# Performance work log

Measured on AMD Instinct MI355X. Metric: run time of the kernel, lower is better.

## Reference

```python
import jax, jax.numpy as jnp
import numpy as np

STFT = 1024
SEQ = 256
CTRL = 32
DEPTH = 3
RATIO = 0.5
BATCH = 64


def _layer_sizes(nin, nout, depth, ratio):
    sizes = []
    for i in range(depth + 1):
        f = i / depth
        lin = nin + (nout - nin) * f
        geo = nin * (nout / nin) ** f
        sizes.append(int(round((1 - ratio) * lin + ratio * geo)))
    sizes[0], sizes[-1] = nin, nout
    return sizes


def _mlp(h, Ws, bs):
    # Linear layers with ReLU between hidden layers, linear final layer.
    n = len(Ws)
    for i in range(n):
        h = h @ Ws[i] + bs[i]
        if i < n - 1:
            h = jax.nn.relu(h)
    return h


def setup_inputs() -> dict:
    key = jax.random.key(0)
    keys = jax.random.split(key, 1 + 4 * DEPTH)
    inp = {"x": jax.random.normal(keys[0], (BATCH, STFT, SEQ), dtype=jnp.float32)}
    enc_sizes = _layer_sizes(1 + 2 * STFT, CTRL, DEPTH, RATIO)
    dec_sizes = _layer_sizes(1 + STFT + CTRL, STFT, DEPTH, RATIO)
    k = 1
    for i in range(DEPTH):
        fan_in = enc_sizes[i]
        inp[f"enc_W{i+1}"] = jax.random.normal(keys[k], (enc_sizes[i], enc_sizes[i + 1]), dtype=jnp.float32) / np.sqrt(fan_in); k += 1
        inp[f"enc_b{i+1}"] = jax.random.normal(keys[k], (enc_sizes[i + 1],), dtype=jnp.float32) * 0.01; k += 1
    for i in range(DEPTH):
        fan_in = dec_sizes[i]
        inp[f"dec_W{i+1}"] = jax.random.normal(keys[k], (dec_sizes[i], dec_sizes[i + 1]), dtype=jnp.float32) / np.sqrt(fan_in); k += 1
        inp[f"dec_b{i+1}"] = jax.random.normal(keys[k], (dec_sizes[i + 1],), dtype=jnp.float32) * 0.01; k += 1
    return inp


def _forward(x, encW, encB, decW, decB):
    B, S, T = x.shape  # [batch, stft_buckets, seq]
    # ---- encode (parallel across t: prev_stft is just the shifted input) ----
    xt = jnp.transpose(x, (0, 2, 1))                       # [B, T, S]
    prev = jnp.concatenate([jnp.zeros((B, 1, S), x.dtype), xt[:, :-1, :]], axis=1)
    tcol = (jnp.arange(T, dtype=x.dtype) / T)[None, :, None]
    tcol = jnp.broadcast_to(tcol, (B, T, 1))
    combined = jnp.concatenate([prev, xt, tcol], axis=-1)  # [B, T, 2S+1]
    controls = _mlp(combined, encW, encB)                  # [B, T, CTRL]
    # ---- decode (true sequential dependency -> scan) ----
    ctrl_t = jnp.transpose(controls, (1, 0, 2))            # [T, B, CTRL]
    tvals = jnp.arange(T, dtype=x.dtype) / T

    def step(prev_stft, xs):
        c, tv = xs
        tc = jnp.broadcast_to(tv, (B, 1))
        comb = jnp.concatenate([c, prev_stft, tc], axis=1)  # [B, CTRL+S+1]
        out = _mlp(comb, decW, decB)                        # [B, S]
        return out, out

    _, recon = jax.lax.scan(step, jnp.zeros((B, S), x.dtype), (ctrl_t, tvals))
    return jnp.transpose(recon, (1, 2, 0))                  # [B, S, T]


def reference(x, enc_W1, enc_b1, enc_W2, enc_b2, enc_W3, enc_b3,
              dec_W1, dec_b1, dec_W2, dec_b2, dec_W3, dec_b3):
    encW = [enc_W1, enc_W2, enc_W3]
    encB = [enc_b1, enc_b2, enc_b3]
    decW = [dec_W1, dec_W2, dec_W3]
    decB = [dec_b1, dec_b2, dec_b3]
    return _forward(x, encW, encB, decW, decB)
```

## Files before the change

### kernel.cpp

```cpp
#include <hip/hip_runtime.h>
#include <cstdint>
#include <cstddef>


#define TT 256
#define BB 64
#define SS 1024

#define EK1 2049
#define EN1 944
#define EN2 416
#define EN3 32

#define DN1 1046
#define DN2 1035
#define DN3 1024

#define KP1 1060
#define KP2 1048
#define KP3 1036
#define NQ1 265
#define NQ2 262
#define NQ3 259
#define WROWS1 1048
#define WROWS2 1040
#define WROWS3 1028

#define OFF_XT    ((size_t)0)
#define OFF_WT1   ((size_t)0)
#define OFF_WT2   ((size_t)1110880)
#define OFF_WT3   ((size_t)2200800)
#define OFF_H1S   ((size_t)3266048)
#define OFF_H2S   ((size_t)20436480)
#define OFF_E1    ((size_t)16777216)
#define OFF_E2    ((size_t)(OFF_E1 + 15466496))
#define OFF_COMB  ((size_t)(OFF_E2 + 6815744))
#define OFF_BAR   ((size_t)(OFF_COMB + 17434880))

#define COMB_SLOT (265 * 256)
#define H1_SLOT   (262 * 256)
#define H2_SLOT   (259 * 256)

typedef unsigned uint4v __attribute__((ext_vector_type(4)));

__global__ void zero_init(float* __restrict__ p, size_t n) {
  size_t i = (size_t)blockIdx.x * blockDim.x + threadIdx.x;
  size_t stride = (size_t)gridDim.x * blockDim.x;
  for (; i < n; i += stride) p[i] = 0.f;
}

__global__ void transpose_x(const float* __restrict__ x, float* __restrict__ xt) {
  __shared__ float tile[32][33];
  int b = blockIdx.z;
  int s0 = blockIdx.x << 5;
  int t0 = blockIdx.y << 5;
  int lt = threadIdx.x & 31;
  int ls = threadIdx.x >> 5;
  const float* xp = x + (size_t)b * SS * TT;
#pragma unroll
  for (int i = 0; i < 4; i++) {
    int s = s0 + ls + (i << 3);
    tile[ls + (i << 3)][lt] = xp[(size_t)s * TT + t0 + lt];
  }
  __syncthreads();
  float* xtp = xt + (size_t)b * TT * SS;
#pragma unroll
  for (int i = 0; i < 4; i++) {
    int t = t0 + ls + (i << 3);
    xtp[(size_t)t * SS + s0 + lt] = tile[lt][ls + (i << 3)];
  }
}

__global__ void transpose_w(const float* __restrict__ W, float* __restrict__ WT,
                            int K, int N, int KPAD, int NCP) {
  __shared__ float tl[32][33];
  int c0 = blockIdx.x << 5, k0 = blockIdx.y << 5;
  int lx = threadIdx.x & 31, ly = threadIdx.x >> 5;
#pragma unroll
  for (int i = 0; i < 4; i++) {
    int k = k0 + ly + (i << 3);
    int c = c0 + lx;
    tl[ly + (i << 3)][lx] = (k < K && c < N) ? W[(size_t)k * N + c] : 0.f;
  }
  __syncthreads();
#pragma unroll
  for (int i = 0; i < 4; i++) {
    int c = c0 + ly + (i << 3);
    int k = k0 + lx;
    if (c < NCP && k < KPAD) WT[(size_t)c * KPAD + k] = tl[lx][ly + (i << 3)];
  }
}

__global__ void init_tail(float* __restrict__ comb) {
  int i = blockIdx.x * blockDim.x + threadIdx.x;
  int t = i >> 6, r = i & 63;
  float4 v;
  v.x = (float)t * (1.f / 256.f);
  v.y = v.z = v.w = 0.f;
  *(float4*)(comb + ((size_t)t * 265 + 264) * 256 + (r << 2)) = v;
}

__device__ inline float4 e1_fetch(const float* __restrict__ xt, int m, int kg) {
  float4 z; z.x = z.y = z.z = z.w = 0.f;
  int t = m & 255;
  if (kg < 1024) {
    if (t == 0) return z;
    return *(const float4*)(xt + (((size_t)(m - 1)) << 10) + kg);
  } else if (kg < 2048) {
    return *(const float4*)(xt + (((size_t)m) << 10) + (kg - 1024));
  } else if (kg == 2048) {
    z.x = (float)t * (1.0f / 256.0f);
    return z;
  }
  return z;
}

template <int AMODE, bool RELU, bool SCATTER>
__global__ __launch_bounds__(256, 2) void gemm_enc(
    const float* __restrict__ A, const float* __restrict__ Bw,
    const float* __restrict__ bias, float* __restrict__ C, int K, int N) {
  __shared__ float As[16][132];
  __shared__ float Bs[16][68];
  const int tid = threadIdx.x;
  const int m0 = blockIdx.x << 7;
  const int n0 = blockIdx.y << 6;
  const int rr = tid >> 4;
  const int cc = tid & 15;
  float acc[8][4];
#pragma unroll
  for (int i = 0; i < 8; i++)
#pragma unroll
    for (int j = 0; j < 4; j++) acc[i][j] = 0.f;

  const int ar = tid >> 2;
  const int akq = (tid & 3) << 2;
  const int bk = tid >> 4;
  const int bn = (tid & 15) << 2;

  for (int k0 = 0; k0 < K; k0 += 16) {
#pragma unroll
    for (int p = 0; p < 2; p++) {
      int m = m0 + ar + (p << 6);
      float4 v;
      if (AMODE == 1) v = e1_fetch(A, m, k0 + akq);
      else            v = *(const float4*)(A + (size_t)m * K + k0 + akq);
      As[akq + 0][ar + (p << 6)] = v.x;
      As[akq + 1][ar + (p << 6)] = v.y;
      As[akq + 2][ar + (p << 6)] = v.z;
      As[akq + 3][ar + (p << 6)] = v.w;
    }
    {
      float4 v; v.x = v.y = v.z = v.w = 0.f;
      if ((k0 + bk) < K && (n0 + bn) < N)
        v = *(const float4*)(Bw + (size_t)(k0 + bk) * N + n0 + bn);
      *(float4*)&Bs[bk][bn] = v;
    }
    __syncthreads();
#pragma unroll
    for (int kk = 0; kk < 16; kk++) {
      float a[8], b4[4];
      *(float4*)&a[0] = *(const float4*)&As[kk][rr << 3];
      *(float4*)&a[4] = *(const float4*)&As[kk][(rr << 3) + 4];
      *(float4*)&b4[0] = *(const float4*)&Bs[kk][cc << 2];
#pragma unroll
      for (int i = 0; i < 8; i++)
#pragma unroll
        for (int j = 0; j < 4; j++) acc[i][j] += a[i] * b4[j];
    }
    __syncthreads();
  }

  if (!SCATTER) {
#pragma unroll
    for (int i = 0; i < 8; i++) {
      int m = m0 + (rr << 3) + i;
      int n = n0 + (cc << 2);
      if (n + 3 < N) {
        float4 o;
        o.x = acc[i][0] + bias[n + 0];
        o.y = acc[i][1] + bias[n + 1];
        o.z = acc[i][2] + bias[n + 2];
        o.w = acc[i][3] + bias[n + 3];
        if (RELU) {
          o.x = fmaxf(o.x, 0.f); o.y = fmaxf(o.y, 0.f);
          o.z = fmaxf(o.z, 0.f); o.w = fmaxf(o.w, 0.f);
        }
        *(float4*)(C + (size_t)m * N + n) = o;
      } else {
#pragma unroll
        for (int j = 0; j < 4; j++) {
          if (n + j < N) {
            float v = acc[i][j] + bias[n + j];
            if (RELU) v = fmaxf(v, 0.f);
            C[(size_t)m * N + n + j] = v;
          }
        }
      }
    }
  } else {
#pragma unroll
    for (int i = 0; i < 8; i++) {
      int m = m0 + (rr << 3) + i;
      int t = m & 255, b = m >> 8;
#pragma unroll
      for (int j = 0; j < 4; j++) {
        int n = n0 + (cc << 2) + j;
        if (n < EN3)
          C[((size_t)t * 265 + (n >> 2)) * 256 + (b << 2) + (n & 3)] = acc[i][j] + bias[n];
      }
    }
  }
}

__device__ inline void gbar(unsigned* __restrict__ bar, unsigned gen, int w) {
  __syncthreads();
  if (threadIdx.x == 0)
    __hip_atomic_store(bar + w, gen, __ATOMIC_RELAXED, __HIP_MEMORY_SCOPE_AGENT);
  if (threadIdx.x < 64) {
    const unsigned* fp = bar + (threadIdx.x << 2);
    for (;;) {
      uint4v f;
      asm volatile(
          "global_load_dwordx4 %0, %1, off sc0 sc1\n\t"
          "s_waitcnt vmcnt(0)"
          : "=v"(f) : "v"(fp));
      if (__all(f.x >= gen && f.y >= gen && f.z >= gen && f.w >= gen)) break;
      __builtin_amdgcn_s_sleep(1);
    }
  }
  __syncthreads();
}

#define DEC_FMA(av, jj)                                              \
  do {                                                               \
    const float* wq = w0 + ((jj) << 2);                              \
    _Pragma("unroll") for (int c = 0; c < NCM; c++) {                \
      float4 wv = *(const float4*)(wq + (size_t)c * KPAD);           \
      acc[c] = fmaf((av).x, wv.x, acc[c]);                           \
      acc[c] = fmaf((av).y, wv.y, acc[c]);                           \
      acc[c] = fmaf((av).z, wv.z, acc[c]);                           \
      acc[c] = fmaf((av).w, wv.w, acc[c]);                           \
    }                                                                \
  } while (0)

template <int NQ, int KPAD, bool RELU, int NCM>
__device__ __forceinline__ void dec_phase(
    const float* __restrict__ actb, const float* __restrict__ wt,
    const float* __restrict__ bias, float* __restrict__ outb, int outk_off,
    int nc, int colbase, int r, int q, float* __restrict__ red, int tid) {
  float acc[NCM];
#pragma unroll
  for (int c = 0; c < NCM; c++) acc[c] = 0.f;
  const float* w0 = wt + (size_t)colbase * KPAD;
  const float* ab = actb + (r << 2);
#pragma unroll 4
  for (int j = q; j < NQ; j += 8) {
    float4 a = *(const float4*)(ab + (j << 8));
    DEC_FMA(a, j);
  }

  float* rp = red + tid * 9;
#pragma unroll
  for (int c = 0; c < NCM; c++) rp[c] = acc[c];
  __syncthreads();
  if (tid < (nc << 6)) {
    int rr = tid / nc;
    int cc = tid - rr * nc;
    float s = 0.f;
#pragma unroll
    for (int q2 = 0; q2 < 8; q2++) s += red[((q2 << 6) + rr) * 9 + cc];
    s += bias[colbase + cc];
    if (RELU) s = fmaxf(s, 0.f);
    int kk = outk_off + colbase + cc;
    __hip_atomic_store(outb + ((size_t)(kk >> 2) << 8) + (rr << 2) + (kk & 3), s,
                       __ATOMIC_RELAXED, __HIP_MEMORY_SCOPE_AGENT);
  }
}

__global__ __launch_bounds__(512, 1) void decoder_kernel(
    const float* __restrict__ wt1, const float* __restrict__ b1,
    const float* __restrict__ wt2, const float* __restrict__ b2,
    const float* __restrict__ wt3, const float* __restrict__ b3,
    float* __restrict__ comb, float* __restrict__ h1s, float* __restrict__ h2s,
    unsigned* __restrict__ bar) {
  __shared__ float red[512 * 9];
  const int tid = threadIdx.x;
  const int w = blockIdx.x;
  const int r = tid & 63;
  const int q = __builtin_amdgcn_readfirstlane(tid >> 6);

  const int nc1 = (w < 22) ? 5 : 4;
  const int cb1 = (w < 22) ? w * 5 : 110 + (w - 22) * 4;
  const int nc2 = (w < 11) ? 5 : 4;
  const int cb2 = (w < 11) ? w * 5 : 55 + (w - 11) * 4;
  const int cb3 = w << 2;

  unsigned gen = 0;
  for (int t = 0; t < TT; t++) {
    gen++; gbar(bar, gen, w);
    dec_phase<NQ1, KP1, true, 5>(comb + (size_t)t * COMB_SLOT, wt1, b1,
                                 h1s + (size_t)t * H1_SLOT, 0,
                                 nc1, cb1, r, q, red, tid);
    gen++; gbar(bar, gen, w);
    dec_phase<NQ2, KP2, true, 5>(h1s + (size_t)t * H1_SLOT, wt2, b2,
                                 h2s + (size_t)t * H2_SLOT, 0,
                                 nc2, cb2, r, q, red, tid);
    gen++; gbar(bar, gen, w);
    dec_phase<NQ3, KP3, false, 4>(h2s + (size_t)t * H2_SLOT, wt3, b3,
                                  comb + (size_t)(t + 1) * COMB_SLOT, 32,
                                  4, cb3, r, q, red, tid);
  }
}

__global__ void permute_out2(const float* __restrict__ comb, float* __restrict__ out) {
  __shared__ float tl[64 * 261];
  int Q = blockIdx.x;
  int t0 = blockIdx.y << 6;
  int tid = threadIdx.x;
  int r = tid & 63, ts = tid >> 6;
#pragma unroll
  for (int i = 0; i < 16; i++) {
    int tt = (i << 2) + ts;
    float4 v = *(const float4*)(comb + ((size_t)(t0 + tt + 1) * 265 + 8 + Q) * 256 + (r << 2));
    float* p = &tl[r * 261];
    p[tt] = v.x; p[65 + tt] = v.y; p[130 + tt] = v.z; p[195 + tt] = v.w;
  }
  __syncthreads();
  int kk = tid & 3, r2 = tid >> 2;
  const float* p = &tl[r2 * 261 + kk * 65];
  float* o = out + ((size_t)r2 * 1024 + (Q << 2) + kk) * 256 + t0;
#pragma unroll
  for (int i = 0; i < 16; i++) {
    int b = i << 2;
    float4 v;
    v.x = p[b]; v.y = p[b + 1]; v.z = p[b + 2]; v.w = p[b + 3];
    *(float4*)(o + b) = v;
  }
}

extern "C" void kernel_launch(void* const* d_in, const int* in_sizes, int n_in,
                              void* d_out, int out_size, void* d_ws, size_t ws_size,
                              hipStream_t stream) {
  (void)in_sizes; (void)n_in; (void)out_size; (void)ws_size;
  const float* x   = (const float*)d_in[0];
  const float* eW1 = (const float*)d_in[1];
  const float* eb1 = (const float*)d_in[2];
  const float* eW2 = (const float*)d_in[3];
  const float* eb2 = (const float*)d_in[4];
  const float* eW3 = (const float*)d_in[5];
  const float* eb3 = (const float*)d_in[6];
  const float* dW1 = (const float*)d_in[7];
  const float* db1 = (const float*)d_in[8];
  const float* dW2 = (const float*)d_in[9];
  const float* db2 = (const float*)d_in[10];
  const float* dW3 = (const float*)d_in[11];
  const float* db3 = (const float*)d_in[12];

  float* ws    = (float*)d_ws;
  float* xt    = ws + OFF_XT;
  float* wt1p  = ws + OFF_WT1;
  float* wt2p  = ws + OFF_WT2;
  float* wt3p  = ws + OFF_WT3;
  float* h1sp  = ws + OFF_H1S;
  float* h2sp  = ws + OFF_H2S;
  float* e1p   = ws + OFF_E1;
  float* e2p   = ws + OFF_E2;
  float* combp = ws + OFF_COMB;
  unsigned* barp = (unsigned*)(ws + OFF_BAR);

  zero_init<<<dim3(64), dim3(256), 0, stream>>>(combp, (size_t)COMB_SLOT);
  zero_init<<<dim3(1), dim3(256), 0, stream>>>((float*)barp, (size_t)2048);

  transpose_x<<<dim3(32, 8, 64), dim3(256), 0, stream>>>(x, xt);

  gemm_enc<1, true,  false><<<dim3(128, 15), dim3(256), 0, stream>>>(xt,  eW1, eb1, e1p, EK1, EN1);
  gemm_enc<0, true,  false><<<dim3(128, 7),  dim3(256), 0, stream>>>(e1p, eW2, eb2, e2p, EN1, EN2);
  gemm_enc<0, false, true ><<<dim3(128, 1),  dim3(256), 0, stream>>>(e2p, eW3, eb3, combp, EN2, EN3);

  transpose_w<<<dim3(33, 34), dim3(256), 0, stream>>>(dW1, wt1p, 1057, DN1, KP1, WROWS1);
  transpose_w<<<dim3(33, 33), dim3(256), 0, stream>>>(dW2, wt2p, 1046, DN2, KP2, WROWS2);
  transpose_w<<<dim3(33, 33), dim3(256), 0, stream>>>(dW3, wt3p, 1035, DN3, KP3, WROWS3);
  init_tail<<<dim3(64), dim3(256), 0, stream>>>(combp);

  const float *a0 = wt1p, *a1 = db1, *a2 = wt2p, *a3 = db2, *a4 = wt3p, *a5 = db3;
  float *r0 = combp, *r1 = h1sp, *r2 = h2sp;
  unsigned* r3 = barp;
  void* kargs[] = {&a0, &a1, &a2, &a3, &a4, &a5, &r0, &r1, &r2, &r3};
  hipLaunchCooperativeKernel((void*)decoder_kernel, dim3(256), dim3(512), kargs,
                             0, stream);

  permute_out2<<<dim3(256, 4), dim3(256), 0, stream>>>(combp, (float*)d_out);
}
```

Baseline: 8.992 ms.

## Repartition decoder work into batch-group by column tiles with LDS-staged activations

```diff
diff --git a/kernel.cpp b/kernel.cpp
--- a/kernel.cpp
+++ b/kernel.cpp
@@ -231,48 +231,68 @@
   __syncthreads();
 }
 
-#define DEC_FMA(av, jj)                                              \
-  do {                                                               \
-    const float* wq = w0 + ((jj) << 2);                              \
-    _Pragma("unroll") for (int c = 0; c < NCM; c++) {                \
-      float4 wv = *(const float4*)(wq + (size_t)c * KPAD);           \
-      acc[c] = fmaf((av).x, wv.x, acc[c]);                           \
-      acc[c] = fmaf((av).y, wv.y, acc[c]);                           \
-      acc[c] = fmaf((av).z, wv.z, acc[c]);                           \
-      acc[c] = fmaf((av).w, wv.w, acc[c]);                           \
-    }                                                                \
-  } while (0)
-
-template <int NQ, int KPAD, bool RELU, int NCM>
+template <int NQ, int KPAD, bool RELU>
 __device__ __forceinline__ void dec_phase(
     const float* __restrict__ actb, const float* __restrict__ wt,
     const float* __restrict__ bias, float* __restrict__ outb, int outk_off,
-    int nc, int colbase, int r, int q, float* __restrict__ red, int tid) {
-  float acc[NCM];
-#pragma unroll
-  for (int c = 0; c < NCM; c++) acc[c] = 0.f;
-  const float* w0 = wt + (size_t)colbase * KPAD;
-  const float* ab = actb + (r << 2);
-#pragma unroll 4
+    int NC, int base, int g, int rloc, int c8, int q,
+    float* __restrict__ lds_act, float* __restrict__ red, int tid) {
+  constexpr int NE = NQ * 8;
+  float4 sv[5];
+#pragma unroll
+  for (int s = 0; s < 5; s++) {
+    int idx = tid + (s << 9);
+    if (idx < NE)
+      sv[s] = *(const float4*)(actb + ((size_t)(idx >> 3) << 8) +
+                               (((g << 3) + (idx & 7)) << 2));
+  }
+#pragma unroll
+  for (int s = 0; s < 5; s++) {
+    int idx = tid + (s << 9);
+    if (idx < NE)
+      *(float4*)(lds_act + ((idx >> 3) << 5) + ((idx & 7) << 2)) = sv[s];
+  }
+  __syncthreads();
+
+  float acc[5];
+#pragma unroll
+  for (int m = 0; m < 5; m++) acc[m] = 0.f;
+  const int NCL = (NC - c8 + 7) >> 3;
+  const float* wb = wt + (size_t)(base + c8) * KPAD;
+#pragma unroll 2
   for (int j = q; j < NQ; j += 8) {
-    float4 a = *(const float4*)(ab + (j << 8));
-    DEC_FMA(a, j);
+    float4 av = *(const float4*)(lds_act + (j << 5) + (rloc << 2));
+    const float* wq = wb + (j << 2);
+#pragma unroll
+    for (int m = 0; m < 5; m++) {
+      if (m < NCL) {
+        float4 wv = *(const float4*)(wq + (size_t)(m << 3) * KPAD);
+        acc[m] = fmaf(av.x, wv.x, acc[m]);
+        acc[m] = fmaf(av.y, wv.y, acc[m]);
+        acc[m] = fmaf(av.z, wv.z, acc[m]);
+        acc[m] = fmaf(av.w, wv.w, acc[m]);
+      }
+    }
   }
 
   float* rp = red + tid * 9;
 #pragma unroll
-  for (int c = 0; c < NCM; c++) rp[c] = acc[c];
-  __syncthreads();
-  if (tid < (nc << 6)) {
-    int rr = tid / nc;
-    int cc = tid - rr * nc;
+  for (int m = 0; m < 5; m++) rp[m] = acc[m];
+  __syncthreads();
+  const int nout = NC << 3;
+  if (tid < nout) {
+    int rr = tid / NC;
+    int ci = tid - rr * NC;
+    int cc8 = ci & 7, cm = ci >> 3;
     float s = 0.f;
 #pragma unroll
-    for (int q2 = 0; q2 < 8; q2++) s += red[((q2 << 6) + rr) * 9 + cc];
-    s += bias[colbase + cc];
+    for (int q2 = 0; q2 < 8; q2++)
+      s += red[((q2 << 6) + (rr << 3) + cc8) * 9 + cm];
+    s += bias[base + ci];
     if (RELU) s = fmaxf(s, 0.f);
-    int kk = outk_off + colbase + cc;
-    __hip_atomic_store(outb + ((size_t)(kk >> 2) << 8) + (rr << 2) + (kk & 3), s,
+    int kk = outk_off + base + ci;
+    int grow = (g << 3) + rr;
+    __hip_atomic_store(outb + ((size_t)(kk >> 2) << 8) + (grow << 2) + (kk & 3), s,
                        __ATOMIC_RELAXED, __HIP_MEMORY_SCOPE_AGENT);
   }
 }
@@ -283,32 +303,37 @@
     const float* __restrict__ wt3, const float* __restrict__ b3,
     float* __restrict__ comb, float* __restrict__ h1s, float* __restrict__ h2s,
     unsigned* __restrict__ bar) {
+  __shared__ float lds_act[265 * 32];
   __shared__ float red[512 * 9];
   const int tid = threadIdx.x;
   const int w = blockIdx.x;
-  const int r = tid & 63;
+  const int g = w >> 5;
+  const int il = w & 31;
+  const int lane = tid & 63;
+  const int rloc = lane >> 3;
+  const int c8 = lane & 7;
   const int q = __builtin_amdgcn_readfirstlane(tid >> 6);
 
-  const int nc1 = (w < 22) ? 5 : 4;
-  const int cb1 = (w < 22) ? w * 5 : 110 + (w - 22) * 4;
-  const int nc2 = (w < 11) ? 5 : 4;
-  const int cb2 = (w < 11) ? w * 5 : 55 + (w - 11) * 4;
-  const int cb3 = w << 2;
+  const int nc1 = (il < 22) ? 33 : 32;
+  const int cb1 = (il < 22) ? il * 33 : 726 + (il - 22) * 32;
+  const int nc2 = (il < 11) ? 33 : 32;
+  const int cb2 = (il < 11) ? il * 33 : 363 + (il - 11) * 32;
+  const int cb3 = il << 5;
 
   unsigned gen = 0;
   for (int t = 0; t < TT; t++) {
     gen++; gbar(bar, gen, w);
-    dec_phase<NQ1, KP1, true, 5>(comb + (size_t)t * COMB_SLOT, wt1, b1,
-                                 h1s + (size_t)t * H1_SLOT, 0,
-                                 nc1, cb1, r, q, red, tid);
+    dec_phase<NQ1, KP1, true>(comb + (size_t)t * COMB_SLOT, wt1, b1,
+                              h1s + (size_t)t * H1_SLOT, 0,
+                              nc1, cb1, g, rloc, c8, q, lds_act, red, tid);
     gen++; gbar(bar, gen, w);
-    dec_phase<NQ2, KP2, true, 5>(h1s + (size_t)t * H1_SLOT, wt2, b2,
-                                 h2s + (size_t)t * H2_SLOT, 0,
-                                 nc2, cb2, r, q, red, tid);
+    dec_phase<NQ2, KP2, true>(h1s + (size_t)t * H1_SLOT, wt2, b2,
+                              h2s + (size_t)t * H2_SLOT, 0,
+                              nc2, cb2, g, rloc, c8, q, lds_act, red, tid);
     gen++; gbar(bar, gen, w);
-    dec_phase<NQ3, KP3, false, 4>(h2s + (size_t)t * H2_SLOT, wt3, b3,
-                                  comb + (size_t)(t + 1) * COMB_SLOT, 32,
-                                  4, cb3, r, q, red, tid);
+    dec_phase<NQ3, KP3, false>(h2s + (size_t)t * H2_SLOT, wt3, b3,
+                               comb + (size_t)(t + 1) * COMB_SLOT, 32,
+                               32, cb3, g, rloc, c8, q, lds_act, red, tid);
   }
 }
 
```

Result: slower. 24.08 ms (+167.8%).
